# Kernel optimization log

Hardware: AMD Instinct MI355X
Metric: run time of the kernel (lower is better)

Reference implementation:

```python
import jax, jax.numpy as jnp
import numpy as np

NSIDE = 128
NPIX = 12 * NSIDE * NSIDE  # 196608
B, C_IN, C_OUT = 8, 16, 32


def setup_inputs() -> dict:
    key = jax.random.key(0)
    k1, k2, k3 = jax.random.split(key, 3)
    x = jax.random.normal(k1, (B, C_IN, NPIX), dtype=jnp.float32)
    # kaiming-normal-like init for Conv1d weight [out, in, 9]
    fan_in = C_IN * 9
    weight = jax.random.normal(k2, (C_OUT, C_IN, 9), dtype=jnp.float32) * jnp.sqrt(2.0 / fan_in)
    b = jnp.zeros((C_OUT,), dtype=jnp.float32)
    # neighbour indices in [0, NPIX]; value NPIX selects the zero-pad column
    neighbours = jax.random.randint(k3, (9 * NPIX,), 0, NPIX + 1, dtype=jnp.int32)
    return {"x": x, "weight": weight, "b": b, "neighbours": neighbours}


def reference(x, weight, b, neighbours):
    # F.pad(x, (0,1)) -> append one zero pixel column so index NPIX reads 0
    x_pad = jnp.pad(x, ((0, 0), (0, 0), (0, 1)))  # [B, C_in, NPIX+1]
    neigh = neighbours.reshape(NPIX, 9)
    # gather: [B, C_in, NPIX, 9]
    vec = x_pad[:, :, neigh]
    # Conv1d(kernel=9, stride=9) over flattened [B,C,9*NPIX] == per-pixel 9-tap contraction
    out = jnp.einsum('bcpk,ock->bop', vec, weight)  # [B, C_out, NPIX]
    return out + b[None, :, None]
```

## Files before the change

### kernel.cpp

```cpp
#include <hip/hip_runtime.h>
#include <hip/hip_bf16.h>

#define NSIDE 128
#define NPIX (12 * NSIDE * NSIDE)
#define BB 8
#define CIN 16
#define COUT 32
#define NROW (NPIX + 1)

typedef _Float16 half8 __attribute__((ext_vector_type(8)));
typedef float floatx16 __attribute__((ext_vector_type(16)));

__global__ __launch_bounds__(256) void prep_xt(const float* __restrict__ x,
                                               _Float16* __restrict__ xt) {
    int r = blockIdx.x * 256 + threadIdx.x;
    const int total = BB * NROW;
    if (r >= total) return;
    int b = r / NROW;
    int p = r - b * NROW;
    half8 lo, hi;
    if (p < NPIX) {
        const float* xp = x + (long)b * CIN * NPIX + p;
#pragma unroll
        for (int c = 0; c < 8; c++) lo[c] = (_Float16)xp[(long)c * NPIX];
#pragma unroll
        for (int c = 0; c < 8; c++) hi[c] = (_Float16)xp[(long)(c + 8) * NPIX];
    } else {
#pragma unroll
        for (int c = 0; c < 8; c++) { lo[c] = (_Float16)0.f; hi[c] = (_Float16)0.f; }
    }
    *(half8*)(xt + (long)r * 16)     = lo;
    *(half8*)(xt + (long)r * 16 + 8) = hi;
}

__global__ __launch_bounds__(256) void prep_wf(const float* __restrict__ w,
                                               _Float16* __restrict__ wf) {
    for (int e = threadIdx.x; e < 9 * 64 * 8; e += 256) {
        int k    = e >> 9;
        int lane = (e >> 3) & 63;
        int j    = e & 7;
        int o    = lane & 31;
        int c    = ((lane >> 5) << 3) + j;
        wf[e] = (_Float16)w[(o * CIN + c) * 9 + k];
    }
}

__global__ __launch_bounds__(256) void conv_main(const _Float16* __restrict__ xt,
                                                 const _Float16* __restrict__ wf,
                                                 const float* __restrict__ bias,
                                                 const int* __restrict__ nb,
                                                 float* __restrict__ out) {
    const int lane  = threadIdx.x & 63;
    const int wv    = threadIdx.x >> 6;
    const int tile  = blockIdx.x * 4 + wv;
    const int b     = tile / (NPIX / 32);
    const int pt    = tile - b * (NPIX / 32);
    const int p     = pt * 32 + (lane & 31);
    const int chalf = (lane >> 5) * 8;

    half8 wfrag[9];
#pragma unroll
    for (int k = 0; k < 9; k++)
        wfrag[k] = *(const half8*)(wf + ((k * 64 + lane) << 3));

    const int* nbp = nb + p * 9;
    int idx[9];
#pragma unroll
    for (int k = 0; k < 9; k++) idx[k] = nbp[k];

    const _Float16* xb = xt + (long)b * NROW * 16 + chalf;
    floatx16 acc;
#pragma unroll
    for (int i = 0; i < 16; i++) acc[i] = 0.f;

#pragma unroll
    for (int k = 0; k < 9; k++) {
        half8 v = *(const half8*)(xb + (long)idx[k] * 16);
        acc = __builtin_amdgcn_mfma_f32_32x32x16_f16(wfrag[k], v, acc, 0, 0, 0);
    }

    float* outb = out + ((long)b * COUT) * NPIX + p;
#pragma unroll
    for (int r = 0; r < 16; r++) {
        int o = (r & 3) + ((r >> 2) << 3) + ((lane >> 5) << 2);
        outb[(long)o * NPIX] = acc[r] + bias[o];
    }
}

extern "C" void kernel_launch(void* const* d_in, const int* in_sizes, int n_in,
                              void* d_out, int out_size, void* d_ws, size_t ws_size,
                              hipStream_t stream) {
    const float* x    = (const float*)d_in[0];
    const float* w    = (const float*)d_in[1];
    const float* bias = (const float*)d_in[2];
    const int*   nb   = (const int*)d_in[3];
    float*       out  = (float*)d_out;

    _Float16* wf = (_Float16*)d_ws;
    _Float16* xt = (_Float16*)((char*)d_ws + 16384);

    int rows = BB * NROW;
    hipLaunchKernelGGL(prep_xt, dim3((rows + 255) / 256), dim3(256), 0, stream, x, xt);
    hipLaunchKernelGGL(prep_wf, dim3(1), dim3(256), 0, stream, w, wf);
    hipLaunchKernelGGL(conv_main, dim3(BB * NPIX / 32 / 4), dim3(256), 0, stream,
                       xt, wf, bias, nb, out);
}
```

Before: 411.6 us.

## Vectorize transpose prep, merge weight prep, interleave batches, use nontemporal accesses

The transpose kernel now makes each thread handle four pixels using float4 loads and writes 16-byte half8 stores, and the weight-fragment prep is folded into the same launch, removing one kernel launch. The main conv kernel maps consecutive blocks to different batches for the same pixel tile, so the neighbour-index reads are shared in cache across batches and gathers stay localized. Streaming loads and stores use nontemporal hints to reduce cache pollution. The risk is that nontemporal loads on the neighbour indices work against the cross-batch reuse the new block mapping is meant to create.

```diff
diff --git a/kernel.cpp b/kernel.cpp
--- a/kernel.cpp
+++ b/kernel.cpp
@@ -1,5 +1,4 @@
 #include <hip/hip_runtime.h>
-#include <hip/hip_bf16.h>
 
 #define NSIDE 128
 #define NPIX (12 * NSIDE * NSIDE)
@@ -10,38 +9,55 @@
 
 typedef _Float16 half8 __attribute__((ext_vector_type(8)));
 typedef float floatx16 __attribute__((ext_vector_type(16)));
+typedef float float4v __attribute__((ext_vector_type(4)));
 
 __global__ __launch_bounds__(256) void prep_xt(const float* __restrict__ x,
-                                               _Float16* __restrict__ xt) {
-    int r = blockIdx.x * 256 + threadIdx.x;
-    const int total = BB * NROW;
-    if (r >= total) return;
-    int b = r / NROW;
-    int p = r - b * NROW;
-    half8 lo, hi;
-    if (p < NPIX) {
-        const float* xp = x + (long)b * CIN * NPIX + p;
+                                               _Float16* __restrict__ xt,
+                                               const float* __restrict__ w,
+                                               _Float16* __restrict__ wf) {
+    const int QPB = NPIX / 4;
+    int t = blockIdx.x * 256 + threadIdx.x;
+    int b = t / QPB;
+    int q = t - b * QPB;
+    long p0 = (long)q * 4;
+
+    const float* xb = x + (long)b * CIN * NPIX + p0;
+    half8 lo[4], hi[4];
 #pragma unroll
-        for (int c = 0; c < 8; c++) lo[c] = (_Float16)xp[(long)c * NPIX];
+    for (int c = 0; c < 8; c++) {
+        float4v v = __builtin_nontemporal_load((const float4v*)(xb + (long)c * NPIX));
 #pragma unroll
-        for (int c = 0; c < 8; c++) hi[c] = (_Float16)xp[(long)(c + 8) * NPIX];
-    } else {
+        for (int i = 0; i < 4; i++) lo[i][c] = (_Float16)v[i];
+    }
 #pragma unroll
-        for (int c = 0; c < 8; c++) { lo[c] = (_Float16)0.f; hi[c] = (_Float16)0.f; }
+    for (int c = 0; c < 8; c++) {
+        float4v v = __builtin_nontemporal_load((const float4v*)(xb + (long)(c + 8) * NPIX));
+#pragma unroll
+        for (int i = 0; i < 4; i++) hi[i][c] = (_Float16)v[i];
     }
-    *(half8*)(xt + (long)r * 16)     = lo;
-    *(half8*)(xt + (long)r * 16 + 8) = hi;
-}
+    half8* dst = (half8*)(xt + ((long)b * NROW + p0) * 16);
+#pragma unroll
+    for (int i = 0; i < 4; i++) {
+        __builtin_nontemporal_store(lo[i], dst + 2 * i);
+        __builtin_nontemporal_store(hi[i], dst + 2 * i + 1);
+    }
 
-__global__ __launch_bounds__(256) void prep_wf(const float* __restrict__ w,
-                                               _Float16* __restrict__ wf) {
-    for (int e = threadIdx.x; e < 9 * 64 * 8; e += 256) {
-        int k    = e >> 9;
-        int lane = (e >> 3) & 63;
-        int j    = e & 7;
-        int o    = lane & 31;
-        int c    = ((lane >> 5) << 3) + j;
-        wf[e] = (_Float16)w[(o * CIN + c) * 9 + k];
+    if (t < BB) {
+        half8 z = (_Float16)0.f;
+        half8* pz = (half8*)(xt + ((long)t * NROW + NPIX) * 16);
+        pz[0] = z;
+        pz[1] = z;
+    }
+
+    if (blockIdx.x == 0) {
+        for (int e = threadIdx.x; e < 9 * 64 * 8; e += 256) {
+            int k    = e >> 9;
+            int lane = (e >> 3) & 63;
+            int j    = e & 7;
+            int o    = lane & 31;
+            int c    = ((lane >> 5) << 3) + j;
+            wf[e] = (_Float16)w[(o * CIN + c) * 9 + k];
+        }
     }
 }
 
@@ -52,9 +68,8 @@
                                                  float* __restrict__ out) {
     const int lane  = threadIdx.x & 63;
     const int wv    = threadIdx.x >> 6;
-    const int tile  = blockIdx.x * 4 + wv;
-    const int b     = tile / (NPIX / 32);
-    const int pt    = tile - b * (NPIX / 32);
+    const int b     = blockIdx.x & 7;
+    const int pt    = (blockIdx.x >> 3) * 4 + wv;
     const int p     = pt * 32 + (lane & 31);
     const int chalf = (lane >> 5) * 8;
 
@@ -66,7 +81,7 @@
     const int* nbp = nb + p * 9;
     int idx[9];
 #pragma unroll
-    for (int k = 0; k < 9; k++) idx[k] = nbp[k];
+    for (int k = 0; k < 9; k++) idx[k] = __builtin_nontemporal_load(nbp + k);
 
     const _Float16* xb = xt + (long)b * NROW * 16 + chalf;
     floatx16 acc;
@@ -80,10 +95,11 @@
     }
 
     float* outb = out + ((long)b * COUT) * NPIX + p;
+    const int obase = (lane >> 5) << 2;
 #pragma unroll
     for (int r = 0; r < 16; r++) {
-        int o = (r & 3) + ((r >> 2) << 3) + ((lane >> 5) << 2);
-        outb[(long)o * NPIX] = acc[r] + bias[o];
+        int o = (r & 3) + ((r >> 2) << 3) + obase;
+        __builtin_nontemporal_store(acc[r] + bias[o], outb + (long)o * NPIX);
     }
 }
 
@@ -99,9 +115,8 @@
     _Float16* wf = (_Float16*)d_ws;
     _Float16* xt = (_Float16*)((char*)d_ws + 16384);
 
-    int rows = BB * NROW;
-    hipLaunchKernelGGL(prep_xt, dim3((rows + 255) / 256), dim3(256), 0, stream, x, xt);
-    hipLaunchKernelGGL(prep_wf, dim3(1), dim3(256), 0, stream, w, wf);
+    hipLaunchKernelGGL(prep_xt, dim3(BB * NPIX / 4 / 256), dim3(256), 0, stream,
+                       x, xt, w, wf);
     hipLaunchKernelGGL(conv_main, dim3(BB * NPIX / 32 / 4), dim3(256), 0, stream,
                        xt, wf, bias, nb, out);
 }
```

Measured after the change: 505.8 us. +22.9%, slower.
